# Performance work log

Measured on AMD Instinct MI355X. Metric: run time of the kernel, lower is better.

Reference implementation:

```python
import jax, jax.numpy as jnp
import numpy as np

N = 100000
E = 3200000
F_IN = 512
HID = 16
C = 40


def setup_inputs() -> dict:
    key = jax.random.key(0)
    ks = jax.random.split(key, 6)
    x = jax.random.normal(ks[0], (N, F_IN), dtype=jnp.float32)
    edge_index = jax.random.randint(ks[1], (2, E), 0, N, dtype=jnp.int64)
    edge_weight = jax.random.uniform(ks[2], (E,), dtype=jnp.float32)
    # Glorot-style init like PyG GCNConv
    W1 = jax.random.normal(ks[3], (F_IN, HID), dtype=jnp.float32) * (1.0 / np.sqrt(F_IN))
    b1 = jnp.zeros((HID,), dtype=jnp.float32)
    W2 = jax.random.normal(ks[4], (HID, C), dtype=jnp.float32) * (1.0 / np.sqrt(HID))
    b2 = jnp.zeros((C,), dtype=jnp.float32)
    return {"x": x, "edge_index": edge_index, "edge_weight": edge_weight,
            "W1": W1, "b1": b1, "W2": W2, "b2": b2}


def _gcn_conv(h, W, b, row, col, norm, num_nodes):
    # h: [N, Fin] -> [N, Fout];  out = D^-1/2 A D^-1/2 (h W) + b, no self loops
    h = h @ W                                           # [N, Fout]
    msg = norm[:, None] * h[row]                        # gather + scale, [E, Fout]
    agg = jax.ops.segment_sum(msg, col, num_segments=num_nodes)  # scatter-add
    return agg + b


def reference(x, edge_index, edge_weight, W1, b1, W2, b2):
    num_nodes = x.shape[0]
    row, col = edge_index[0], edge_index[1]
    # symmetric gcn normalization (add_self_loops=False)
    deg = jax.ops.segment_sum(edge_weight, col, num_segments=num_nodes)  # [N]
    deg_inv_sqrt = jnp.where(deg > 0, jax.lax.rsqrt(jnp.maximum(deg, 1e-30)), 0.0)
    norm = deg_inv_sqrt[row] * edge_weight * deg_inv_sqrt[col]           # [E]

    h = jax.nn.relu(_gcn_conv(x, W1, b1, row, col, norm, num_nodes))
    # dropout is identity in eval mode (training=False)
    h = _gcn_conv(h, W2, b2, row, col, norm, num_nodes)
    return jax.nn.log_softmax(h, axis=-1)
```

## Files before the change

### kernel.cpp

```cpp
#include <hip/hip_runtime.h>

typedef float floatx4_t __attribute__((ext_vector_type(4)));
typedef __bf16 bf16x8_t __attribute__((ext_vector_type(8)));
typedef short shortx8_t __attribute__((ext_vector_type(8)));
typedef unsigned long long ull;

__device__ __forceinline__ unsigned short f2bf_rne(float f) {
    unsigned u = __float_as_uint(f);
    unsigned r = u + 0x7FFFu + ((u >> 16) & 1u);
    return (unsigned short)(r >> 16);
}
__device__ __forceinline__ float bf2f(unsigned short h) {
    return __uint_as_float((unsigned)h << 16);
}

#define MAXB 2048
#define CHUNK 8192
#define CAP 3072

__global__ __launch_bounds__(256) void k_scatter_gemm(const int* __restrict__ row,
                                                      const int* __restrict__ col,
                                                      const float* __restrict__ ew,
                                                      int* __restrict__ gcnt,
                                                      ull* __restrict__ packed,
                                                      const float* __restrict__ x,
                                                      const float* __restrict__ W1,
                                                      float* __restrict__ h1f,
                                                      int E, int B, int gC, int N) {
    int t = threadIdx.x;
    if ((int)blockIdx.x < gC) {
        __shared__ int h[MAXB];
        __shared__ int base[MAXB];
        for (int i = t; i < B; i += 256) h[i] = 0;
        __syncthreads();
        int cbase = blockIdx.x * CHUNK;
#pragma unroll 2
        for (int k = 0; k < 8; ++k) {
            int e = cbase + k * 1024 + t * 4;
            if (e + 3 < E) {
                int4 c4 = *(const int4*)(col + e);
                atomicAdd(&h[c4.x >> 6], 1);
                atomicAdd(&h[c4.y >> 6], 1);
                atomicAdd(&h[c4.z >> 6], 1);
                atomicAdd(&h[c4.w >> 6], 1);
            } else {
                for (int j = 0; j < 4; ++j)
                    if (e + j < E) atomicAdd(&h[col[e + j] >> 6], 1);
            }
        }
        __syncthreads();
        for (int i = t; i < B; i += 256) {
            int c = h[i];
            base[i] = c ? atomicAdd(&gcnt[i], c) : 0;
        }
        __syncthreads();
#pragma unroll 2
        for (int k = 0; k < 8; ++k) {
            int e = cbase + k * 1024 + t * 4;
            if (e + 3 < E) {
                int4 c4 = *(const int4*)(col + e);
                int4 r4 = *(const int4*)(row + e);
                float4 w4 = *(const float4*)(ew + e);
                int cs[4] = {c4.x, c4.y, c4.z, c4.w};
                int rs[4] = {r4.x, r4.y, r4.z, r4.w};
                float wsv[4] = {w4.x, w4.y, w4.z, w4.w};
#pragma unroll
                for (int j = 0; j < 4; ++j) {
                    int c = cs[j];
                    int b = c >> 6;
                    int pos = atomicAdd(&base[b], 1);
                    if (pos < CAP) {
                        ull hi = (ull)(unsigned)((rs[j] << 6) | (c & 63)) << 32;
                        packed[(size_t)b * CAP + pos] = hi | (unsigned)__float_as_uint(wsv[j]);
                    }
                }
            } else {
                for (int j = 0; j < 4; ++j) {
                    if (e + j < E) {
                        int c = col[e + j];
                        int b = c >> 6;
                        int pos = atomicAdd(&base[b], 1);
                        if (pos < CAP) {
                            ull hi = (ull)(unsigned)((row[e + j] << 6) | (c & 63)) << 32;
                            packed[(size_t)b * CAP + pos] = hi | (unsigned)__float_as_uint(ew[e + j]);
                        }
                    }
                }
            }
        }
    } else {
        int b = blockIdx.x - gC;
        const int lane = t & 63;
        const int wave = t >> 6;
        const int m = lane & 15;
        const int q = lane >> 4;
        const int nbase = b * 64 + wave * 16;

        shortx8_t bs[16];
#pragma unroll
        for (int c = 0; c < 16; ++c) {
#pragma unroll
            for (int j = 0; j < 8; ++j) {
                int k = c * 32 + q * 8 + j;
                bs[c][j] = (short)f2bf_rne(W1[k * 16 + m]);
            }
        }

        int rowi = nbase + m;
        if (rowi >= N) rowi = N - 1;
        const float* xr = x + (size_t)rowi * 512;

        floatx4_t acc = {0.f, 0.f, 0.f, 0.f};
#pragma unroll
        for (int c = 0; c < 16; ++c) {
            const float4 u0 = *(const float4*)(xr + c * 32 + q * 8);
            const float4 u1 = *(const float4*)(xr + c * 32 + q * 8 + 4);
            shortx8_t as;
            as[0] = (short)f2bf_rne(u0.x); as[1] = (short)f2bf_rne(u0.y);
            as[2] = (short)f2bf_rne(u0.z); as[3] = (short)f2bf_rne(u0.w);
            as[4] = (short)f2bf_rne(u1.x); as[5] = (short)f2bf_rne(u1.y);
            as[6] = (short)f2bf_rne(u1.z); as[7] = (short)f2bf_rne(u1.w);
            acc = __builtin_amdgcn_mfma_f32_16x16x32_bf16(
                __builtin_bit_cast(bf16x8_t, as),
                __builtin_bit_cast(bf16x8_t, bs[c]), acc, 0, 0, 0);
        }

#pragma unroll
        for (int r = 0; r < 4; ++r) {
            int node = nbase + q * 4 + r;
            if (node < N)
                h1f[(size_t)node * 16 + m] = acc[r];
        }
    }
}

__global__ __launch_bounds__(256) void k_sortdis(const int* __restrict__ gcnt,
                                                 const ull* __restrict__ packed,
                                                 unsigned* __restrict__ packed2,
                                                 int2* __restrict__ rng,
                                                 float* __restrict__ dis,
                                                 const float* __restrict__ h1f,
                                                 unsigned short* __restrict__ h1s, int N) {
    __shared__ ull stage[CAP];
    __shared__ unsigned s2[CAP];
    __shared__ int cnt4[4][64];
    __shared__ float dacc4[4][64];
    __shared__ int cur[64];
    __shared__ float sdis[64];
    __shared__ int stot;
    int t = threadIdx.x;
    int w4 = t >> 6;
    if (t < 64) {
#pragma unroll
        for (int s = 0; s < 4; ++s) { cnt4[s][t] = 0; dacc4[s][t] = 0.f; }
    }
    __syncthreads();
    int b = blockIdx.x;
    size_t gbase = (size_t)b * CAP;
    int szr = gcnt[b];
    int sz = szr < CAP ? szr : CAP;

    for (int j = t; j < sz; j += 256) stage[j] = packed[gbase + j];
    for (int j = t; j < CAP; j += 256) s2[j] = 0u;
    __syncthreads();

    for (int j = t; j < sz; j += 256) {
        ull p = stage[j];
        int nd = (int)(p >> 32) & 63;
        atomicAdd(&cnt4[w4][nd], 1);
        atomicAdd(&dacc4[w4][nd], __uint_as_float((unsigned)p));
    }
    __syncthreads();
    if (t < 64) {
        int c = (cnt4[0][t] + cnt4[1][t]) + (cnt4[2][t] + cnt4[3][t]);
        float s = (dacc4[0][t] + dacc4[1][t]) + (dacc4[2][t] + dacc4[3][t]);
        int cpad = (c + 3) & ~3;
        int xp = cpad;
#pragma unroll
        for (int off = 1; off < 64; off <<= 1) {
            int y = __shfl_up(xp, off);
            if (t >= off) xp += y;
        }
        int off0 = xp - cpad;
        cur[t] = off0;
        if (t == 63) stot = xp;
        float d = (s > 0.f) ? rsqrtf(s) : 0.f;
        sdis[t] = d;
        int g = b * 64 + t;
        if (g < N) {
            int o0 = off0 < CAP ? off0 : CAP;
            int e1 = off0 + c; e1 = e1 < CAP ? e1 : CAP;
            rng[g] = make_int2((int)gbase + o0, (int)gbase + e1);
            dis[g] = d;
        }
    }
    __syncthreads();
    for (int j = t; j < sz; j += 256) {
        ull p = stage[j];
        int hi = (int)(p >> 32);
        int nd = hi & 63;
        int r = hi >> 6;
        unsigned short wb = f2bf_rne(__uint_as_float((unsigned)p));
        int pos = atomicAdd(&cur[nd], 1);
        if (pos < CAP) s2[pos] = ((unsigned)r << 15) | (unsigned)wb;
    }
    __syncthreads();
    int szp = stot < CAP ? stot : CAP;
    for (int j = t; j < szp; j += 256) packed2[gbase + j] = s2[j];
    for (int k = t; k < 1024; k += 256) {
        int n = k >> 4, f = k & 15;
        int node = b * 64 + n;
        if (node < N) {
            size_t idx = (size_t)node * 16 + f;
            h1s[idx] = f2bf_rne(sdis[n] * h1f[idx]);
        }
    }
}

__global__ __launch_bounds__(256) void k_agg1(const int2* __restrict__ rng,
                                              const unsigned* __restrict__ packed2,
                                              const float* __restrict__ dis,
                                              const unsigned short* __restrict__ h1s,
                                              const float* __restrict__ b1,
                                              unsigned short* __restrict__ hs, int N) {
    int wv = (blockIdx.x * 256 + threadIdx.x) >> 6;
    if (wv >= N) return;
    int lane = threadIdx.x & 63;
    int e4 = lane >> 4, f = lane & 15;
    int2 r2 = rng[wv];
    int beg = r2.x, end = r2.y;
    float a0 = 0.f, a1 = 0.f, a2 = 0.f, a3 = 0.f;
    for (int i = beg + e4 * 4; i < end; i += 16) {
        uint4 p4 = *(const uint4*)(packed2 + i);
        int r0 = p4.x >> 15, r1 = p4.y >> 15, r2i = p4.z >> 15, r3 = p4.w >> 15;
        a0 += __uint_as_float((p4.x & 0x7FFFu) << 16) * bf2f(h1s[(size_t)r0 * 16 + f]);
        a1 += __uint_as_float((p4.y & 0x7FFFu) << 16) * bf2f(h1s[(size_t)r1 * 16 + f]);
        a2 += __uint_as_float((p4.z & 0x7FFFu) << 16) * bf2f(h1s[(size_t)r2i * 16 + f]);
        a3 += __uint_as_float((p4.w & 0x7FFFu) << 16) * bf2f(h1s[(size_t)r3 * 16 + f]);
    }
    float a = (a0 + a1) + (a2 + a3);
    a += __shfl_xor(a, 16);
    a += __shfl_xor(a, 32);
    if (e4 == 0) {
        float dg = dis[wv];
        float v = dg * a + b1[f];
        v = (v > 0.f) ? v : 0.f;
        hs[(size_t)wv * 16 + f] = f2bf_rne(dg * v);
    }
}

__global__ __launch_bounds__(256) void k_agg2out(const int2* __restrict__ rng,
                                                 const unsigned* __restrict__ packed2,
                                                 const float* __restrict__ dis,
                                                 const unsigned short* __restrict__ hs,
                                                 const float* __restrict__ W2,
                                                 const float* __restrict__ b2,
                                                 float* __restrict__ out, int N) {
    int wv = (blockIdx.x * 256 + threadIdx.x) >> 6;
    if (wv >= N) return;
    int lane = threadIdx.x & 63;
    int e4 = lane >> 4, f = lane & 15;
    int2 r2 = rng[wv];
    int beg = r2.x, end = r2.y;
    float a0 = 0.f, a1 = 0.f, a2 = 0.f, a3 = 0.f;
    for (int i = beg + e4 * 4; i < end; i += 16) {
        uint4 p4 = *(const uint4*)(packed2 + i);
        int r0 = p4.x >> 15, r1 = p4.y >> 15, r2i = p4.z >> 15, r3 = p4.w >> 15;
        a0 += __uint_as_float((p4.x & 0x7FFFu) << 16) * bf2f(hs[(size_t)r0 * 16 + f]);
        a1 += __uint_as_float((p4.y & 0x7FFFu) << 16) * bf2f(hs[(size_t)r1 * 16 + f]);
        a2 += __uint_as_float((p4.z & 0x7FFFu) << 16) * bf2f(hs[(size_t)r2i * 16 + f]);
        a3 += __uint_as_float((p4.w & 0x7FFFu) << 16) * bf2f(hs[(size_t)r3 * 16 + f]);
    }
    float a = (a0 + a1) + (a2 + a3);
    a += __shfl_xor(a, 16);
    a += __shfl_xor(a, 32);

    float dg = dis[wv];
    int c = lane;
    int cc = (c < 40) ? c : 39;
    float z = 0.f;
#pragma unroll
    for (int fi = 0; fi < 16; ++fi) {
        float af = __shfl(a, fi);
        z += af * W2[fi * 40 + cc];
    }
    z = dg * z + b2[cc];

    float zm = (c < 40) ? z : -3.4e38f;
#pragma unroll
    for (int off = 1; off < 64; off <<= 1) zm = fmaxf(zm, __shfl_xor(zm, off));
    float ex = (c < 40) ? __expf(z - zm) : 0.f;
    float s = ex;
#pragma unroll
    for (int off = 1; off < 64; off <<= 1) s += __shfl_xor(s, off);
    float lse = zm + __logf(s);
    if (c < 40) out[(size_t)wv * 40 + c] = z - lse;
}

extern "C" void kernel_launch(void* const* d_in, const int* in_sizes, int n_in,
                              void* d_out, int out_size, void* d_ws, size_t ws_size,
                              hipStream_t stream) {
    const float* x  = (const float*)d_in[0];
    const int*   ei = (const int*)d_in[1];
    const float* ew = (const float*)d_in[2];
    const float* W1 = (const float*)d_in[3];
    const float* b1 = (const float*)d_in[4];
    const float* W2 = (const float*)d_in[5];
    const float* b2 = (const float*)d_in[6];

    const int N = in_sizes[0] / 512;
    const int E = in_sizes[2];
    const int* row = ei;
    const int* col = ei + E;
    const int B = (N + 63) >> 6;
    const int Npad = B * 64;

    ull*      packed  = (ull*)d_ws;
    unsigned* packed2 = (unsigned*)(packed + (size_t)B * CAP);
    int*      gcnt    = (int*)(packed2 + (size_t)B * CAP);
    int2*     rng     = (int2*)(gcnt + B + (B & 1));
    float*    dis     = (float*)(rng + N);
    float*    h1f     = dis + N;
    unsigned short* h1s = (unsigned short*)(h1f + (size_t)16 * Npad);
    unsigned short* hs  = h1s + (size_t)16 * Npad;

    hipMemsetAsync(gcnt, 0, (size_t)B * sizeof(int), stream);

    const int gC = (E + CHUNK - 1) / CHUNK;
    const int gW = (N * 64 + 255) / 256;

    k_scatter_gemm<<<gC + B, 256, 0, stream>>>(row, col, ew, gcnt, packed,
                                               x, W1, h1f, E, B, gC, N);
    k_sortdis<<<B, 256, 0, stream>>>(gcnt, packed, packed2, rng, dis, h1f, h1s, N);
    k_agg1<<<gW, 256, 0, stream>>>(rng, packed2, dis, h1s, b1, hs, N);
    k_agg2out<<<gW, 256, 0, stream>>>(rng, packed2, dis, hs, W2, b2, (float*)d_out, N);
}
```

Before: 494.7 us.

## Stage edge chunk in shared memory to read edge arrays once

Result: slower. 508.7 us (+2.8%).

```diff
diff --git a/kernel.cpp b/kernel.cpp
--- a/kernel.cpp
+++ b/kernel.cpp
@@ -15,7 +15,7 @@
 }
 
 #define MAXB 2048
-#define CHUNK 8192
+#define CHUNK 4096
 #define CAP 3072
 
 __global__ __launch_bounds__(256) void k_scatter_gemm(const int* __restrict__ row,
@@ -29,34 +29,17 @@
                                                       int E, int B, int gC, int N) {
     int t = threadIdx.x;
     if ((int)blockIdx.x < gC) {
-        __shared__ int h[MAXB];
-        __shared__ int base[MAXB];
-        for (int i = t; i < B; i += 256) h[i] = 0;
+        __shared__ int hb[MAXB];
+        __shared__ ull stage[CHUNK];
+        __shared__ unsigned short sbuck[CHUNK];
+        for (int i = t; i < B; i += 256) hb[i] = 0;
         __syncthreads();
         int cbase = blockIdx.x * CHUNK;
+        int nloc = E - cbase; if (nloc > CHUNK) nloc = CHUNK;
 #pragma unroll 2
-        for (int k = 0; k < 8; ++k) {
-            int e = cbase + k * 1024 + t * 4;
-            if (e + 3 < E) {
-                int4 c4 = *(const int4*)(col + e);
-                atomicAdd(&h[c4.x >> 6], 1);
-                atomicAdd(&h[c4.y >> 6], 1);
-                atomicAdd(&h[c4.z >> 6], 1);
-                atomicAdd(&h[c4.w >> 6], 1);
-            } else {
-                for (int j = 0; j < 4; ++j)
-                    if (e + j < E) atomicAdd(&h[col[e + j] >> 6], 1);
-            }
-        }
-        __syncthreads();
-        for (int i = t; i < B; i += 256) {
-            int c = h[i];
-            base[i] = c ? atomicAdd(&gcnt[i], c) : 0;
-        }
-        __syncthreads();
-#pragma unroll 2
-        for (int k = 0; k < 8; ++k) {
-            int e = cbase + k * 1024 + t * 4;
+        for (int k = 0; k < 4; ++k) {
+            int l = k * 1024 + t * 4;
+            int e = cbase + l;
             if (e + 3 < E) {
                 int4 c4 = *(const int4*)(col + e);
                 int4 r4 = *(const int4*)(row + e);
@@ -68,25 +51,34 @@
                 for (int j = 0; j < 4; ++j) {
                     int c = cs[j];
                     int b = c >> 6;
-                    int pos = atomicAdd(&base[b], 1);
-                    if (pos < CAP) {
-                        ull hi = (ull)(unsigned)((rs[j] << 6) | (c & 63)) << 32;
-                        packed[(size_t)b * CAP + pos] = hi | (unsigned)__float_as_uint(wsv[j]);
-                    }
+                    atomicAdd(&hb[b], 1);
+                    stage[l + j] = ((ull)(unsigned)((rs[j] << 6) | (c & 63)) << 32)
+                                   | (unsigned)__float_as_uint(wsv[j]);
+                    sbuck[l + j] = (unsigned short)b;
                 }
             } else {
                 for (int j = 0; j < 4; ++j) {
                     if (e + j < E) {
                         int c = col[e + j];
                         int b = c >> 6;
-                        int pos = atomicAdd(&base[b], 1);
-                        if (pos < CAP) {
-                            ull hi = (ull)(unsigned)((row[e + j] << 6) | (c & 63)) << 32;
-                            packed[(size_t)b * CAP + pos] = hi | (unsigned)__float_as_uint(ew[e + j]);
-                        }
+                        atomicAdd(&hb[b], 1);
+                        stage[l + j] = ((ull)(unsigned)((row[e + j] << 6) | (c & 63)) << 32)
+                                       | (unsigned)__float_as_uint(ew[e + j]);
+                        sbuck[l + j] = (unsigned short)b;
                     }
                 }
             }
+        }
+        __syncthreads();
+        for (int i = t; i < B; i += 256) {
+            int c = hb[i];
+            hb[i] = c ? atomicAdd(&gcnt[i], c) : 0;
+        }
+        __syncthreads();
+        for (int l = t; l < nloc; l += 256) {
+            int b = sbuck[l];
+            int pos = atomicAdd(&hb[b], 1);
+            if (pos < CAP) packed[(size_t)b * CAP + pos] = stage[l];
         }
     } else {
         int b = blockIdx.x - gC;
```

## Widen column buckets to 128 nodes and drop LDS staging in sort pass

Applied to the files above, without the earlier changes.

Measured after the change: 489.0 us. Within noise of the previous version (-1.2%).

```diff
diff --git a/kernel.cpp b/kernel.cpp
--- a/kernel.cpp
+++ b/kernel.cpp
@@ -14,9 +14,9 @@
     return __uint_as_float((unsigned)h << 16);
 }
 
-#define MAXB 2048
+#define MAXB2 1024
 #define CHUNK 8192
-#define CAP 3072
+#define CAP2 6144
 
 __global__ __launch_bounds__(256) void k_scatter_gemm(const int* __restrict__ row,
                                                       const int* __restrict__ col,
@@ -26,12 +26,12 @@
                                                       const float* __restrict__ x,
                                                       const float* __restrict__ W1,
                                                       float* __restrict__ h1f,
-                                                      int E, int B, int gC, int N) {
+                                                      int E, int B2, int gC, int N) {
     int t = threadIdx.x;
     if ((int)blockIdx.x < gC) {
-        __shared__ int h[MAXB];
-        __shared__ int base[MAXB];
-        for (int i = t; i < B; i += 256) h[i] = 0;
+        __shared__ int h[MAXB2];
+        __shared__ int base[MAXB2];
+        for (int i = t; i < B2; i += 256) h[i] = 0;
         __syncthreads();
         int cbase = blockIdx.x * CHUNK;
 #pragma unroll 2
@@ -39,17 +39,17 @@
             int e = cbase + k * 1024 + t * 4;
             if (e + 3 < E) {
                 int4 c4 = *(const int4*)(col + e);
-                atomicAdd(&h[c4.x >> 6], 1);
-                atomicAdd(&h[c4.y >> 6], 1);
-                atomicAdd(&h[c4.z >> 6], 1);
-                atomicAdd(&h[c4.w >> 6], 1);
+                atomicAdd(&h[c4.x >> 7], 1);
+                atomicAdd(&h[c4.y >> 7], 1);
+                atomicAdd(&h[c4.z >> 7], 1);
+                atomicAdd(&h[c4.w >> 7], 1);
             } else {
                 for (int j = 0; j < 4; ++j)
-                    if (e + j < E) atomicAdd(&h[col[e + j] >> 6], 1);
+                    if (e + j < E) atomicAdd(&h[col[e + j] >> 7], 1);
             }
         }
         __syncthreads();
-        for (int i = t; i < B; i += 256) {
+        for (int i = t; i < B2; i += 256) {
             int c = h[i];
             base[i] = c ? atomicAdd(&gcnt[i], c) : 0;
         }
@@ -67,22 +67,22 @@
 #pragma unroll
                 for (int j = 0; j < 4; ++j) {
                     int c = cs[j];
-                    int b = c >> 6;
+                    int b = c >> 7;
                     int pos = atomicAdd(&base[b], 1);
-                    if (pos < CAP) {
-                        ull hi = (ull)(unsigned)((rs[j] << 6) | (c & 63)) << 32;
-                        packed[(size_t)b * CAP + pos] = hi | (unsigned)__float_as_uint(wsv[j]);
+                    if (pos < CAP2) {
+                        ull hi = (ull)(unsigned)((rs[j] << 7) | (c & 127)) << 32;
+                        packed[(size_t)b * CAP2 + pos] = hi | (unsigned)__float_as_uint(wsv[j]);
                     }
                 }
             } else {
                 for (int j = 0; j < 4; ++j) {
                     if (e + j < E) {
                         int c = col[e + j];
-                        int b = c >> 6;
+                        int b = c >> 7;
                         int pos = atomicAdd(&base[b], 1);
-                        if (pos < CAP) {
-                            ull hi = (ull)(unsigned)((row[e + j] << 6) | (c & 63)) << 32;
-                            packed[(size_t)b * CAP + pos] = hi | (unsigned)__float_as_uint(ew[e + j]);
+                        if (pos < CAP2) {
+                            ull hi = (ull)(unsigned)((row[e + j] << 7) | (c & 127)) << 32;
+                            packed[(size_t)b * CAP2 + pos] = hi | (unsigned)__float_as_uint(ew[e + j]);
                         }
                     }
                 }
@@ -141,75 +141,78 @@
                                                  float* __restrict__ dis,
                                                  const float* __restrict__ h1f,
                                                  unsigned short* __restrict__ h1s, int N) {
-    __shared__ ull stage[CAP];
-    __shared__ unsigned s2[CAP];
-    __shared__ int cnt4[4][64];
-    __shared__ float dacc4[4][64];
-    __shared__ int cur[64];
-    __shared__ float sdis[64];
-    __shared__ int stot;
+    __shared__ unsigned s2[CAP2];
+    __shared__ int cnt4[4][128];
+    __shared__ float dacc4[4][128];
+    __shared__ int cur[128];
+    __shared__ float sdis[128];
+    __shared__ int htot[2];
     int t = threadIdx.x;
     int w4 = t >> 6;
-    if (t < 64) {
+    int lane = t & 63;
+    if (t < 128) {
 #pragma unroll
         for (int s = 0; s < 4; ++s) { cnt4[s][t] = 0; dacc4[s][t] = 0.f; }
     }
+    for (int j = t; j < CAP2; j += 256) s2[j] = 0u;
     __syncthreads();
     int b = blockIdx.x;
-    size_t gbase = (size_t)b * CAP;
+    size_t gbase = (size_t)b * CAP2;
     int szr = gcnt[b];
-    int sz = szr < CAP ? szr : CAP;
-
-    for (int j = t; j < sz; j += 256) stage[j] = packed[gbase + j];
-    for (int j = t; j < CAP; j += 256) s2[j] = 0u;
-    __syncthreads();
+    int sz = szr < CAP2 ? szr : CAP2;
 
     for (int j = t; j < sz; j += 256) {
-        ull p = stage[j];
-        int nd = (int)(p >> 32) & 63;
+        ull p = packed[gbase + j];
+        int nd = (int)(p >> 32) & 127;
         atomicAdd(&cnt4[w4][nd], 1);
         atomicAdd(&dacc4[w4][nd], __uint_as_float((unsigned)p));
     }
     __syncthreads();
-    if (t < 64) {
-        int c = (cnt4[0][t] + cnt4[1][t]) + (cnt4[2][t] + cnt4[3][t]);
-        float s = (dacc4[0][t] + dacc4[1][t]) + (dacc4[2][t] + dacc4[3][t]);
-        int cpad = (c + 3) & ~3;
-        int xp = cpad;
+    int c = 0, cpad = 0, xp = 0;
+    float s = 0.f;
+    if (t < 128) {
+        c = (cnt4[0][t] + cnt4[1][t]) + (cnt4[2][t] + cnt4[3][t]);
+        s = (dacc4[0][t] + dacc4[1][t]) + (dacc4[2][t] + dacc4[3][t]);
+        cpad = (c + 3) & ~3;
+        xp = cpad;
 #pragma unroll
         for (int off = 1; off < 64; off <<= 1) {
             int y = __shfl_up(xp, off);
-            if (t >= off) xp += y;
-        }
-        int off0 = xp - cpad;
+            if (lane >= off) xp += y;
+        }
+        if (lane == 63) htot[t >> 6] = xp;
+    }
+    __syncthreads();
+    if (t < 128) {
+        int off0 = xp - cpad + ((t >= 64) ? htot[0] : 0);
         cur[t] = off0;
-        if (t == 63) stot = xp;
         float d = (s > 0.f) ? rsqrtf(s) : 0.f;
         sdis[t] = d;
-        int g = b * 64 + t;
+        int g = b * 128 + t;
         if (g < N) {
-            int o0 = off0 < CAP ? off0 : CAP;
-            int e1 = off0 + c; e1 = e1 < CAP ? e1 : CAP;
+            int o0 = off0 < CAP2 ? off0 : CAP2;
+            int e1 = off0 + c; e1 = e1 < CAP2 ? e1 : CAP2;
             rng[g] = make_int2((int)gbase + o0, (int)gbase + e1);
             dis[g] = d;
         }
     }
     __syncthreads();
     for (int j = t; j < sz; j += 256) {
-        ull p = stage[j];
+        ull p = packed[gbase + j];
         int hi = (int)(p >> 32);
-        int nd = hi & 63;
-        int r = hi >> 6;
+        int nd = hi & 127;
+        int r = hi >> 7;
         unsigned short wb = f2bf_rne(__uint_as_float((unsigned)p));
         int pos = atomicAdd(&cur[nd], 1);
-        if (pos < CAP) s2[pos] = ((unsigned)r << 15) | (unsigned)wb;
-    }
-    __syncthreads();
-    int szp = stot < CAP ? stot : CAP;
+        if (pos < CAP2) s2[pos] = ((unsigned)r << 15) | (unsigned)wb;
+    }
+    __syncthreads();
+    int stot = htot[0] + htot[1];
+    int szp = stot < CAP2 ? stot : CAP2;
     for (int j = t; j < szp; j += 256) packed2[gbase + j] = s2[j];
-    for (int k = t; k < 1024; k += 256) {
+    for (int k = t; k < 2048; k += 256) {
         int n = k >> 4, f = k & 15;
-        int node = b * 64 + n;
+        int node = b * 128 + n;
         if (node < N) {
             size_t idx = (size_t)node * 16 + f;
             h1s[idx] = f2bf_rne(sdis[n] * h1f[idx]);
@@ -312,26 +315,27 @@
     const int E = in_sizes[2];
     const int* row = ei;
     const int* col = ei + E;
-    const int B = (N + 63) >> 6;
-    const int Npad = B * 64;
+    const int B2 = (N + 127) >> 7;
+    const int Bg = (N + 63) >> 6;
+    const int Npad = Bg * 64;
 
     ull*      packed  = (ull*)d_ws;
-    unsigned* packed2 = (unsigned*)(packed + (size_t)B * CAP);
-    int*      gcnt    = (int*)(packed2 + (size_t)B * CAP);
-    int2*     rng     = (int2*)(gcnt + B + (B & 1));
+    unsigned* packed2 = (unsigned*)(packed + (size_t)B2 * CAP2);
+    int*      gcnt    = (int*)(packed2 + (size_t)B2 * CAP2);
+    int2*     rng     = (int2*)(gcnt + B2 + (B2 & 1));
     float*    dis     = (float*)(rng + N);
     float*    h1f     = dis + N;
     unsigned short* h1s = (unsigned short*)(h1f + (size_t)16 * Npad);
     unsigned short* hs  = h1s + (size_t)16 * Npad;
 
-    hipMemsetAsync(gcnt, 0, (size_t)B * sizeof(int), stream);
+    hipMemsetAsync(gcnt, 0, (size_t)B2 * sizeof(int), stream);
 
     const int gC = (E + CHUNK - 1) / CHUNK;
     const int gW = (N * 64 + 255) / 256;
 
-    k_scatter_gemm<<<gC + B, 256, 0, stream>>>(row, col, ew, gcnt, packed,
-                                               x, W1, h1f, E, B, gC, N);
-    k_sortdis<<<B, 256, 0, stream>>>(gcnt, packed, packed2, rng, dis, h1f, h1s, N);
+    k_scatter_gemm<<<gC + Bg, 256, 0, stream>>>(row, col, ew, gcnt, packed,
+                                                x, W1, h1f, E, B2, gC, N);
+    k_sortdis<<<B2, 256, 0, stream>>>(gcnt, packed, packed2, rng, dis, h1f, h1s, N);
     k_agg1<<<gW, 256, 0, stream>>>(rng, packed2, dis, h1s, b1, hs, N);
     k_agg2out<<<gW, 256, 0, stream>>>(rng, packed2, dis, hs, W2, b2, (float*)d_out, N);
 }
```
